# Kernel optimization log

Measured on AMD Instinct MI355X. Metric: run time of the kernel, lower is better.

Reference implementation:

```python
import jax, jax.numpy as jnp
import numpy as np

B, NCLS, NHEADS, CIN, CPROJ = 2, 24, 8, 1024, 128
D0, H0, W0 = 4, 6, 8
KS, EPS = 4, 1e-5


def _bn_relu(x, g, b):
    # training-mode BatchNorm3d (biased var over N,D,H,W) + ReLU
    m = x.mean((0, 2, 3, 4), keepdims=True)
    v = x.var((0, 2, 3, 4), keepdims=True)
    y = (x - m) * jax.lax.rsqrt(v + EPS)
    y = y * g[None, :, None, None, None] + b[None, :, None, None, None]
    return jax.nn.relu(y)


def _convt(x, w, b):
    # torch ConvTranspose3d(k=4, stride=2, pad=1); w: [Cin, Cout, 4,4,4]
    wf = jnp.flip(w, (2, 3, 4)).transpose(1, 0, 2, 3, 4)  # -> [Cout, Cin, k,k,k]
    y = jax.lax.conv_general_dilated(
        x, wf, window_strides=(1, 1, 1),
        padding=[(KS - 1 - 1, KS - 1 - 1)] * 3,  # k-1-p = 2
        lhs_dilation=(2, 2, 2),
        dimension_numbers=("NCDHW", "OIDHW", "NCDHW"))
    return y + b[None, :, None, None, None]


def setup_inputs() -> dict:
    key = jax.random.key(0)
    ks = jax.random.split(key, 20)
    f32 = jnp.float32
    inp = {
        "x_in": jax.random.normal(ks[0], (B, CIN, D0, H0, W0), f32),
        "y_in": jax.random.normal(ks[1], (B, NCLS), f32),
        # multi-headed lookup tables: [n_heads, n_classes, 1*1*1*Cin*Cout]
        "tables": jax.random.normal(ks[2], (NHEADS, NCLS, CIN * CPROJ), f32) * 0.02,
        # BN affine params (gamma init 1, beta init 0 like torch)
        "g0": jnp.ones((1024,), f32), "be0": jnp.zeros((1024,), f32),
        "g1": jnp.ones((512,), f32), "be1": jnp.zeros((512,), f32),
        "g2": jnp.ones((256,), f32), "be2": jnp.zeros((256,), f32),
        "g3": jnp.ones((128,), f32), "be3": jnp.zeros((128,), f32),
        "g4": jnp.ones((32,), f32), "be4": jnp.zeros((32,), f32),
        # ConvTranspose3d weights [Cin, Cout, k, k, k] and biases
        "w1": jax.random.normal(ks[3], (1024, 512, KS, KS, KS), f32) * 0.01,
        "b1": jnp.zeros((512,), f32),
        "w2": jax.random.normal(ks[4], (512, 256, KS, KS, KS), f32) * 0.01,
        "b2": jnp.zeros((256,), f32),
        "w3": jax.random.normal(ks[5], (256, 128, KS, KS, KS), f32) * 0.01,
        "b3": jnp.zeros((128,), f32),
        "w4": jax.random.normal(ks[6], (128, 32, KS, KS, KS), f32) * 0.01,
        "b4": jnp.zeros((32,), f32),
        "w5": jax.random.normal(ks[7], (32, 1, KS, KS, KS), f32) * 0.01,
        "b5": jnp.zeros((1,), f32),
    }
    return inp


def reference(x_in, y_in, tables, g0, be0, g1, be1, g2, be2, g3, be3, g4, be4,
              w1, b1, w2, b2, w3, b3, w4, b4, w5, b5):
    # hypernetwork: per-sample per-head 1x1x1 conv weights
    w = jnp.einsum("bq,hqk->bhk", y_in, tables)
    w = w.reshape(B, NHEADS, CPROJ, CIN)  # [B,H,Cout,Cin]
    # dynamic 1x1x1 conv3d over all samples/heads in one batched contraction
    x = jnp.einsum("bcxyz,bhoc->bhoxyz", x_in, w)
    x = x.reshape(B, NHEADS * CPROJ, D0, H0, W0)  # heads concatenated on channels
    # decoder stack
    x = _bn_relu(x, g0, be0)
    x = _convt(x, w1, b1)
    x = _bn_relu(x, g1, be1)
    x = _convt(x, w2, b2)
    x = _bn_relu(x, g2, be2)
    x = _convt(x, w3, b3)
    x = _bn_relu(x, g3, be3)
    x = _convt(x, w4, b4)
    x = _bn_relu(x, g4, be4)
    x = _convt(x, w5, b5)
    return jax.nn.sigmoid(x)  # [B, 1, 128, 192, 256]
```

## Files before the change

kernel.cpp:

```cpp
#include <hip/hip_runtime.h>
#include <hip/hip_bf16.h>
#include <math.h>

typedef __attribute__((ext_vector_type(8))) short short8;
typedef __attribute__((ext_vector_type(4))) float f32x4;

__device__ __forceinline__ unsigned short f2bf(float f) {
    unsigned u = __builtin_bit_cast(unsigned, f);
    return (unsigned short)((u + 0x7fffu + ((u >> 16) & 1u)) >> 16);
}
__device__ __forceinline__ float bf2f(unsigned short h) {
    unsigned u = ((unsigned)h) << 16;
    return __builtin_bit_cast(float, u);
}

static constexpr int NCLS_ = 24;

__global__ void hyper_k(const float* __restrict__ y, const float* __restrict__ tables,
                        float* __restrict__ wproj) {
    int idx = blockIdx.x * 256 + threadIdx.x;
    int h = idx >> 17;
    int k = idx & 131071;
    const float* t = tables + (size_t)h * NCLS_ * 131072 + k;
    float a0 = 0.f, a1 = 0.f;
#pragma unroll
    for (int q = 0; q < NCLS_; q++) {
        float v = t[(size_t)q << 17];
        a0 = fmaf(y[q], v, a0);
        a1 = fmaf(y[NCLS_ + q], v, a1);
    }
    wproj[idx] = a0;
    wproj[(1u << 20) + idx] = a1;
}

__global__ void conv0_k(const float* __restrict__ xin, const float* __restrict__ wp,
                        unsigned short* __restrict__ x0) {
    int o = blockIdx.x, b = blockIdx.y;
    __shared__ float wl[1024];
    for (int i = threadIdx.x; i < 1024; i += 256)
        wl[i] = wp[((size_t)b << 20) + (size_t)o * 1024 + i];
    __syncthreads();
    int s = threadIdx.x;
    if (s < 192) {
        const float* xb = xin + (size_t)b * 1024 * 192 + s;
        float acc = 0.f;
#pragma unroll 8
        for (int c = 0; c < 1024; c++) acc = fmaf(xb[(size_t)c * 192], wl[c], acc);
        int z = s / 48, rem = s - z * 48, yy = rem / 8, xx = rem - yy * 8;
        int pi = ((z & 1) << 2) | ((yy & 1) << 1) | (xx & 1);
        int qi = ((z >> 1) * 3 + (yy >> 1)) * 4 + (xx >> 1);
        x0[(((size_t)pi * 2 + b) * 24 + qi) * 1024 + o] = f2bf(acc);
    }
}

template <int CO, int CI>
__global__ void wt_k(const float* __restrict__ W, unsigned short* __restrict__ Wt) {
    int t = blockIdx.x * 256 + threadIdx.x;
    int p = t / (CO * CI);
    int rem = t - p * (CO * CI);
    int co = rem / CI;
    int rem2 = rem - co * CI;
    int ci_hi = rem2 >> 3, j = rem2 & 7;
    int pz = p >> 2, py = (p >> 1) & 1, px = p & 1;
    int jz = j >> 2, jy = (j >> 1) & 1, jx = j & 1;
    int tap = (1 - pz + 2 * jz) * 16 + (1 - py + 2 * jy) * 4 + (1 - px + 2 * jx);
    short8 ov;
#pragma unroll
    for (int cl = 0; cl < 8; cl++) {
        float v = W[((size_t)(ci_hi * 8 + cl) * CO + co) * 64 + tap];
        ov[cl] = (short)f2bf(v);
    }
    *(short8*)(Wt + ((size_t)(p * CO + co) * (CI * 8) + ci_hi * 64 + j * 8)) = ov;
}

template <int C>
__global__ __launch_bounds__(256) void bnstats3_k(const unsigned short* __restrict__ x,
                                                  float* __restrict__ sums, int R) {
    constexpr int G = C / 8;
    constexpr int REP = 256 / G;
    const int t = threadIdx.x;
    const int g = t % G;
    const int rep = t / G;
    float s1[8], s2[8];
#pragma unroll
    for (int k = 0; k < 8; k++) { s1[k] = 0.f; s2[k] = 0.f; }
    for (int r = blockIdx.x * REP + rep; r < R; r += gridDim.x * REP) {
        short8 v = *(const short8*)(x + (size_t)r * C + g * 8);
#pragma unroll
        for (int k = 0; k < 8; k++) {
            float f = bf2f((unsigned short)v[k]);
            s1[k] += f;
            s2[k] = fmaf(f, f, s2[k]);
        }
    }
    __shared__ float red[2][256][8];
#pragma unroll
    for (int k = 0; k < 8; k++) { red[0][t][k] = s1[k]; red[1][t][k] = s2[k]; }
    __syncthreads();
#pragma unroll
    for (int step = 128; step >= 1; step >>= 1) {
        if (step >= G) {
            if (t < step) {
#pragma unroll
                for (int k = 0; k < 8; k++) {
                    red[0][t][k] += red[0][t + step][k];
                    red[1][t][k] += red[1][t + step][k];
                }
            }
            __syncthreads();
        }
    }
    if (t < G) {
#pragma unroll
        for (int k = 0; k < 8; k++) {
            atomicAdd(&sums[t * 8 + k], red[0][t][k]);
            atomicAdd(&sums[C + t * 8 + k], red[1][t][k]);
        }
    }
}

__global__ void bnfinal_k(const float* __restrict__ sums, const float* __restrict__ g,
                          const float* __restrict__ be, float* __restrict__ sc,
                          float* __restrict__ sh, int C, float invN) {
    int c = blockIdx.x * 256 + threadIdx.x;
    if (c < C) {
        float m = sums[c] * invN;
        float v = sums[C + c] * invN - m * m;
        float s = g[c] * rsqrtf(v + 1e-5f);
        sc[c] = s;
        sh[c] = be[c] - m * s;
    }
}

__global__ void bnapply2_k(unsigned short* __restrict__ x, const float* __restrict__ sc,
                           const float* __restrict__ sh, int C, int total8) {
    int i = blockIdx.x * 256 + threadIdx.x;
    if (i >= total8) return;
    int c0 = (i * 8) % C;
    short8 v = *(short8*)(x + (size_t)i * 8);
    short8 ov;
#pragma unroll
    for (int k = 0; k < 8; k++) {
        float f = bf2f((unsigned short)v[k]);
        f = fmaxf(0.f, fmaf(f, sc[c0 + k], sh[c0 + k]));
        ov[k] = (short)f2bf(f);
    }
    *(short8*)(x + (size_t)i * 8) = ov;
}

template <int CO, int CI, int DI, int HI, int WI, int TZ, int TY, int TX, int WM, int BMW, bool SIG>
__global__ __launch_bounds__(256) void convt_mfma(const unsigned short* __restrict__ xin,
                                                  const unsigned short* __restrict__ Wt,
                                                  const float* __restrict__ bias,
                                                  void* __restrict__ xout) {
    constexpr int WN = 4 / WM;
    constexpr int WTZ = TZ / WN, WTY = TY, WTX = TX;
    constexpr int LWTX = (WTX == 8) ? 3 : ((WTX == 4) ? 2 : 1);
    constexpr int LWTY = (WTY == 4) ? 2 : ((WTY == 2) ? 1 : 0);
    constexpr int YS = TX + 1;
    constexpr int ZS = (TY + 1) * (TX + 1);
    constexpr int WINR = (TZ + 1) * ZS;
    constexpr int AROWS = WM * BMW;
    constexpr int MT = (CO + BMW * WM - 1) / (BMW * WM);
    constexpr int MF = BMW / 16;
    constexpr int KT = CI / 8;
    constexpr int HH = HI / 2, WH = WI / 2;
    constexpr int SQI = (DI / 2) * HH * WH;
    constexpr int SQO = DI * HI * WI;
    constexpr int WITER = (WINR + 255) / 256;
    constexpr int AITER = (AROWS * 8 + 255) / 256;

    __shared__ short lw[WINR * 8];
    __shared__ short la[AROWS * 72];

    const int tid = threadIdx.x;
    const int mt = blockIdx.x % MT;
    const int nt = blockIdx.x / MT;
    constexpr int NTX = WI / TX, NTY = HI / TY;
    const int tx = nt % NTX;
    const int tyz = nt / NTX;
    const int ty = tyz % NTY;
    const int tz = tyz / NTY;
    const int q0z = tz * TZ, q0y = ty * TY, q0x = tx * TX;
    const int p = blockIdx.y;
    const int pz = p >> 2, py = (p >> 1) & 1, px = p & 1;
    const int b = blockIdx.z;

    const unsigned short* srcp[WITER];
    int dstw[WITER];
#pragma unroll
    for (int rr = 0; rr < WITER; rr++) {
        int row = tid + rr * 256;
        srcp[rr] = nullptr;
        dstw[rr] = row * 8;
        if (row < WINR) {
            int wz = row / ZS;
            int rm = row - wz * ZS;
            int wy = rm / YS;
            int wx = rm - wy * YS;
            int gz = q0z + pz - 1 + wz, gy = q0y + py - 1 + wy, gx = q0x + px - 1 + wx;
            if ((unsigned)gz < (unsigned)DI && (unsigned)gy < (unsigned)HI &&
                (unsigned)gx < (unsigned)WI) {
                int pin = ((gz & 1) << 2) | ((gy & 1) << 1) | (gx & 1);
                int qin = ((gz >> 1) * HH + (gy >> 1)) * WH + (gx >> 1);
                srcp[rr] = xin + (((size_t)pin * 2 + b) * SQI + qin) * CI;
            }
        }
    }
    const unsigned short* asrc[AITER];
    int dsta[AITER];
#pragma unroll
    for (int ar = 0; ar < AITER; ar++) {
        int t2 = tid + ar * 256;
        asrc[ar] = nullptr;
        dsta[ar] = 0;
        if (t2 < AROWS * 8) {
            int row = t2 >> 3, seg = t2 & 7;
            int co = mt * (BMW * WM) + row;
            dsta[ar] = row * 72 + seg * 8;
            if (co < CO) asrc[ar] = Wt + (size_t)(p * CO + co) * (CI * 8) + seg * 8;
        }
    }

    const int lane = tid & 63;
    const int r15 = lane & 15, l4 = lane >> 4;
    const int w = tid >> 6;
    const int wm = (WM == 4) ? w : 0;
    const int wn = (WM == 4) ? 0 : w;
    const int jy = (l4 >> 1) & 1, jx = l4 & 1;

    int baddr[4];
#pragma unroll
    for (int nf = 0; nf < 4; nf++) {
        int n = nf * 16 + r15;
        int qx = n & (WTX - 1);
        int qy = (n >> LWTX) & (WTY - 1);
        int qz = (n >> (LWTX + LWTY)) + wn * WTZ;
        baddr[nf] = ((qz + 1) * ZS + (qy + 1 - jy) * YS + (qx + 1 - jx)) * 8;
    }

    f32x4 acc[MF][4];
#pragma unroll
    for (int mf = 0; mf < MF; mf++) {
        int cobase = mt * (BMW * WM) + wm * BMW + mf * 16 + l4 * 4;
        f32x4 bv;
#pragma unroll
        for (int r = 0; r < 4; r++) bv[r] = (cobase + r < CO) ? bias[cobase + r] : 0.f;
#pragma unroll
        for (int nf = 0; nf < 4; nf++) acc[mf][nf] = bv;
    }

    for (int kt = 0; kt < KT; kt++) {
        __syncthreads();
#pragma unroll
        for (int rr = 0; rr < WITER; rr++) {
            int row = tid + rr * 256;
            if ((WINR % 256 == 0) || row < WINR) {
                short8 v = {0, 0, 0, 0, 0, 0, 0, 0};
                if (srcp[rr]) v = *(const short8*)(srcp[rr] + kt * 8);
                *(short8*)(lw + dstw[rr]) = v;
            }
        }
#pragma unroll
        for (int ar = 0; ar < AITER; ar++) {
            int t2 = tid + ar * 256;
            if (((AROWS * 8) % 256 == 0) || t2 < AROWS * 8) {
                short8 v = {0, 0, 0, 0, 0, 0, 0, 0};
                if (asrc[ar]) v = *(const short8*)(asrc[ar] + kt * 64);
                *(short8*)(la + dsta[ar]) = v;
            }
        }
        __syncthreads();

        short8 af[MF][2], bfr[4][2];
#pragma unroll
        for (int mf = 0; mf < MF; mf++)
#pragma unroll
            for (int ks = 0; ks < 2; ks++)
                af[mf][ks] =
                    *(const short8*)(la + (wm * BMW + mf * 16 + r15) * 72 + ks * 32 + l4 * 8);
#pragma unroll
        for (int nf = 0; nf < 4; nf++)
#pragma unroll
            for (int ks = 0; ks < 2; ks++)
                bfr[nf][ks] = *(const short8*)(lw + baddr[nf] - ks * (ZS * 8));
#pragma unroll
        for (int mf = 0; mf < MF; mf++)
#pragma unroll
            for (int nf = 0; nf < 4; nf++)
#pragma unroll
                for (int ks = 0; ks < 2; ks++)
                    acc[mf][nf] = __builtin_amdgcn_mfma_f32_16x16x32_bf16(
                        af[mf][ks], bfr[nf][ks], acc[mf][nf], 0, 0, 0);
    }

#pragma unroll
    for (int nf = 0; nf < 4; nf++) {
        int n = nf * 16 + r15;
        int qx = q0x + (n & (WTX - 1));
        int qy = q0y + ((n >> LWTX) & (WTY - 1));
        int qz = q0z + (n >> (LWTX + LWTY)) + wn * WTZ;
        if constexpr (SIG) {
            if (l4 == 0) {
                int oz = 2 * qz + pz, oy = 2 * qy + py, ox = 2 * qx + px;
                float v = acc[0][nf][0];
                v = 1.f / (1.f + __expf(-v));
                ((float*)xout)[(size_t)b * (8 * SQO) + ((size_t)oz * (2 * HI) + oy) * (2 * WI) +
                               ox] = v;
            }
        } else {
            int gq = (qz * HI + qy) * WI + qx;
#pragma unroll
            for (int mf = 0; mf < MF; mf++) {
                int cobase = mt * (BMW * WM) + wm * BMW + mf * 16 + l4 * 4;
                unsigned long long pk = 0;
#pragma unroll
                for (int r = 0; r < 4; r++)
                    pk |= (unsigned long long)f2bf(acc[mf][nf][r]) << (16 * r);
                *(unsigned long long*)((unsigned short*)xout +
                                       (((size_t)p * 2 + b) * SQO + gq) * CO + cobase) = pk;
            }
        }
    }
}

extern "C" void kernel_launch(void* const* d_in, const int* in_sizes, int n_in,
                              void* d_out, int out_size, void* d_ws, size_t ws_size,
                              hipStream_t stream) {
    const float* x_in = (const float*)d_in[0];
    const float* y_in = (const float*)d_in[1];
    const float* tables = (const float*)d_in[2];
    const float* g0 = (const float*)d_in[3];
    const float* be0 = (const float*)d_in[4];
    const float* g1 = (const float*)d_in[5];
    const float* be1 = (const float*)d_in[6];
    const float* g2 = (const float*)d_in[7];
    const float* be2 = (const float*)d_in[8];
    const float* g3 = (const float*)d_in[9];
    const float* be3 = (const float*)d_in[10];
    const float* g4 = (const float*)d_in[11];
    const float* be4 = (const float*)d_in[12];
    const float* w1 = (const float*)d_in[13];
    const float* b1 = (const float*)d_in[14];
    const float* w2 = (const float*)d_in[15];
    const float* b2 = (const float*)d_in[16];
    const float* w3 = (const float*)d_in[17];
    const float* b3 = (const float*)d_in[18];
    const float* w4 = (const float*)d_in[19];
    const float* b4 = (const float*)d_in[20];
    const float* w5 = (const float*)d_in[21];
    const float* b5 = (const float*)d_in[22];
    float* out = (float*)d_out;

    char* base = (char*)d_ws;
    size_t off = 0;
    auto alloc = [&](size_t bytes) -> void* {
        void* r = base + off;
        off += (bytes + 255) & ~(size_t)255;
        return r;
    };
    float* wproj = (float*)alloc(8388608);
    unsigned short* x0 = (unsigned short*)alloc(786432);
    unsigned short* x1 = (unsigned short*)alloc(3145728);
    unsigned short* x2 = (unsigned short*)alloc(12582912);
    unsigned short* x3 = (unsigned short*)alloc(50331648);
    unsigned short* x4 = (unsigned short*)alloc(100663296);
    unsigned short* Wt1 = (unsigned short*)alloc(67108864);
    unsigned short* Wt2 = (unsigned short*)alloc(16777216);
    unsigned short* Wt3 = (unsigned short*)alloc(4194304);
    unsigned short* Wt4 = (unsigned short*)alloc(524288);
    unsigned short* Wt5 = (unsigned short*)alloc(4096);
    float* sums = (float*)alloc(8192);
    float* sc = (float*)alloc(4096);
    float* sh = (float*)alloc(4096);

    hyper_k<<<4096, 256, 0, stream>>>(y_in, tables, wproj);
    conv0_k<<<dim3(1024, 2), 256, 0, stream>>>(x_in, wproj, x0);

    wt_k<512, 1024><<<16384, 256, 0, stream>>>(w1, Wt1);
    wt_k<256, 512><<<4096, 256, 0, stream>>>(w2, Wt2);
    wt_k<128, 256><<<1024, 256, 0, stream>>>(w3, Wt3);
    wt_k<32, 128><<<128, 256, 0, stream>>>(w4, Wt4);
    wt_k<1, 32><<<1, 256, 0, stream>>>(w5, Wt5);

    hipMemsetAsync(sums, 0, 2 * 1024 * 4, stream);
    bnstats3_k<1024><<<192, 256, 0, stream>>>(x0, sums, 384);
    bnfinal_k<<<4, 256, 0, stream>>>(sums, g0, be0, sc, sh, 1024, 1.f / 384);
    bnapply2_k<<<192, 256, 0, stream>>>(x0, sc, sh, 1024, 49152);
    convt_mfma<512, 1024, 4, 6, 8, 4, 2, 8, 4, 32, false>
        <<<dim3(12, 8, 2), 256, 0, stream>>>(x0, Wt1, b1, x1);

    hipMemsetAsync(sums, 0, 2 * 512 * 4, stream);
    bnstats3_k<512><<<512, 256, 0, stream>>>(x1, sums, 3072);
    bnfinal_k<<<2, 256, 0, stream>>>(sums, g1, be1, sc, sh, 512, 1.f / 3072);
    bnapply2_k<<<768, 256, 0, stream>>>(x1, sc, sh, 512, 196608);
    convt_mfma<256, 512, 8, 12, 16, 8, 4, 8, 1, 32, false>
        <<<dim3(48, 8, 2), 256, 0, stream>>>(x1, Wt2, b2, x2);

    hipMemsetAsync(sums, 0, 2 * 256 * 4, stream);
    bnstats3_k<256><<<512, 256, 0, stream>>>(x2, sums, 24576);
    bnfinal_k<<<1, 256, 0, stream>>>(sums, g2, be2, sc, sh, 256, 1.f / 24576);
    bnapply2_k<<<3072, 256, 0, stream>>>(x2, sc, sh, 256, 786432);
    convt_mfma<128, 256, 16, 24, 32, 8, 4, 8, 1, 32, false>
        <<<dim3(192, 8, 2), 256, 0, stream>>>(x2, Wt3, b3, x3);

    hipMemsetAsync(sums, 0, 2 * 128 * 4, stream);
    bnstats3_k<128><<<512, 256, 0, stream>>>(x3, sums, 196608);
    bnfinal_k<<<1, 256, 0, stream>>>(sums, g3, be3, sc, sh, 128, 1.f / 196608);
    bnapply2_k<<<12288, 256, 0, stream>>>(x3, sc, sh, 128, 3145728);
    convt_mfma<32, 128, 32, 48, 64, 8, 4, 8, 1, 32, false>
        <<<dim3(384, 8, 2), 256, 0, stream>>>(x3, Wt4, b4, x4);

    hipMemsetAsync(sums, 0, 2 * 32 * 4, stream);
    bnstats3_k<32><<<512, 256, 0, stream>>>(x4, sums, 1572864);
    bnfinal_k<<<1, 256, 0, stream>>>(sums, g4, be4, sc, sh, 32, 1.f / 1572864);
    bnapply2_k<<<24576, 256, 0, stream>>>(x4, sc, sh, 32, 6291456);
    convt_mfma<1, 32, 64, 96, 128, 8, 4, 8, 1, 16, true>
        <<<dim3(3072, 8, 2), 256, 0, stream>>>(x4, Wt5, b5, out);
}
```

Measured before the change: 2.283 ms.

## Add all-parity convt kernel sharing one input window for the last two layers

Adds convt_mfma2, which stages a single halo input window (TZ+2 x TY+2 x TX+2 voxels, 8 channels per step) into LDS and has each of the four waves compute two of the eight output parities from it. Before, each parity was a separate grid slice that reloaded its own input. Layers 4 and 5 now use this kernel, which is aimed at the redundant input reads and the launch overhead of per-parity blocks. In exchange it syncs twice per 8-channel K step with tiny LDS stages, and the final sigmoid layer still wastes most of each MFMA on a single output channel.

```diff
diff --git a/kernel.cpp b/kernel.cpp
--- a/kernel.cpp
+++ b/kernel.cpp
@@ -300,25 +300,170 @@
         int qx = q0x + (n & (WTX - 1));
         int qy = q0y + ((n >> LWTX) & (WTY - 1));
         int qz = q0z + (n >> (LWTX + LWTY)) + wn * WTZ;
-        if constexpr (SIG) {
-            if (l4 == 0) {
-                int oz = 2 * qz + pz, oy = 2 * qy + py, ox = 2 * qx + px;
-                float v = acc[0][nf][0];
-                v = 1.f / (1.f + __expf(-v));
-                ((float*)xout)[(size_t)b * (8 * SQO) + ((size_t)oz * (2 * HI) + oy) * (2 * WI) +
-                               ox] = v;
-            }
-        } else {
-            int gq = (qz * HI + qy) * WI + qx;
+        int gq = (qz * HI + qy) * WI + qx;
+#pragma unroll
+        for (int mf = 0; mf < MF; mf++) {
+            int cobase = mt * (BMW * WM) + wm * BMW + mf * 16 + l4 * 4;
+            unsigned long long pk = 0;
+#pragma unroll
+            for (int r = 0; r < 4; r++)
+                pk |= (unsigned long long)f2bf(acc[mf][nf][r]) << (16 * r);
+            *(unsigned long long*)((unsigned short*)xout +
+                                   (((size_t)p * 2 + b) * SQO + gq) * CO + cobase) = pk;
+        }
+    }
+}
+
+template <int CO, int CI, int DI, int HI, int WI, int TZ, int TY, int TX, int BM, bool SIG>
+__global__ __launch_bounds__(256) void convt_mfma2(const unsigned short* __restrict__ xin,
+                                                   const unsigned short* __restrict__ Wt,
+                                                   const float* __restrict__ bias,
+                                                   void* __restrict__ xout) {
+    constexpr int WZ = TZ + 2, WY = TY + 2, WX = TX + 2;
+    constexpr int WINR = WZ * WY * WX;
+    constexpr int TQ = TZ * TY * TX;
+    constexpr int SF = TQ / 16;
+    constexpr int MF = BM / 16;
+    constexpr int MT = (CO + BM - 1) / BM;
+    constexpr int KT = CI / 8;
+    constexpr int HH = HI / 2, WH = WI / 2;
+    constexpr int SQI = (DI / 2) * HH * WH;
+    constexpr int SQO = DI * HI * WI;
+    static_assert(WINR <= 256, "window must fit one staging pass");
+
+    __shared__ short lw[WINR * 8];
+
+    const int tid = threadIdx.x;
+    const int bx = blockIdx.x;
+    const int mt = bx % MT;
+    const int tile = bx / MT;
+    constexpr int NTX = WI / TX, NTY = HI / TY;
+    const int tx = tile % NTX;
+    const int tyz = tile / NTX;
+    const int ty = tyz % NTY;
+    const int tz = tyz / NTY;
+    const int b = blockIdx.y;
+
+    const unsigned short* srcw = nullptr;
+    if (tid < WINR) {
+        int wz = tid / (WY * WX);
+        int rm = tid - wz * (WY * WX);
+        int wy = rm / WX;
+        int wx = rm - wy * WX;
+        int gz = tz * TZ - 1 + wz, gy = ty * TY - 1 + wy, gx = tx * TX - 1 + wx;
+        if ((unsigned)gz < (unsigned)DI && (unsigned)gy < (unsigned)HI &&
+            (unsigned)gx < (unsigned)WI) {
+            int pin = ((gz & 1) << 2) | ((gy & 1) << 1) | (gx & 1);
+            int qin = ((gz >> 1) * HH + (gy >> 1)) * WH + (gx >> 1);
+            srcw = xin + (((size_t)pin * 2 + b) * SQI + qin) * CI;
+        }
+    }
+
+    const int lane = tid & 63;
+    const int r15 = lane & 15, l4 = lane >> 4;
+    const int w = tid >> 6;
+    const int jy = (l4 >> 1) & 1, jx = l4 & 1;
+
+    const unsigned short* aptr[2][MF];
+#pragma unroll
+    for (int pp = 0; pp < 2; pp++) {
+        int p = 2 * w + pp;
+#pragma unroll
+        for (int mf = 0; mf < MF; mf++) {
+            int co = mt * BM + mf * 16 + r15;
+            if (co >= CO) co = CO - 1;
+            aptr[pp][mf] = Wt + ((size_t)p * CO + co) * (CI * 8) + l4 * 8;
+        }
+    }
+
+    int poff[2];
+#pragma unroll
+    for (int pp = 0; pp < 2; pp++) {
+        int p = 2 * w + pp;
+        poff[pp] = ((p >> 2) * WY + ((p >> 1) & 1)) * WX + (p & 1);
+    }
+    int baddr0[SF];
+#pragma unroll
+    for (int sf = 0; sf < SF; sf++) {
+        int s = sf * 16 + r15;
+        int qxr = s % TX, qyr = (s / TX) % TY, qzr = s / (TX * TY);
+        baddr0[sf] = ((qzr + 1) * WY + (qyr + 1 - jy)) * WX + (qxr + 1 - jx);
+    }
+
+    f32x4 acc[MF][2 * SF];
+#pragma unroll
+    for (int mf = 0; mf < MF; mf++) {
+        int cobase = mt * BM + mf * 16 + l4 * 4;
+        f32x4 bv;
+#pragma unroll
+        for (int r = 0; r < 4; r++) bv[r] = (cobase + r < CO) ? bias[cobase + r] : 0.f;
+#pragma unroll
+        for (int nf = 0; nf < 2 * SF; nf++) acc[mf][nf] = bv;
+    }
+
+    for (int kt = 0; kt < KT; kt++) {
+        __syncthreads();
+        if (tid < WINR) {
+            short8 v = {0, 0, 0, 0, 0, 0, 0, 0};
+            if (srcw) v = *(const short8*)(srcw + kt * 8);
+            *(short8*)(lw + tid * 8) = v;
+        }
+        short8 af[2][MF][2];
+#pragma unroll
+        for (int pp = 0; pp < 2; pp++)
 #pragma unroll
             for (int mf = 0; mf < MF; mf++) {
-                int cobase = mt * (BMW * WM) + wm * BMW + mf * 16 + l4 * 4;
-                unsigned long long pk = 0;
-#pragma unroll
-                for (int r = 0; r < 4; r++)
-                    pk |= (unsigned long long)f2bf(acc[mf][nf][r]) << (16 * r);
-                *(unsigned long long*)((unsigned short*)xout +
-                                       (((size_t)p * 2 + b) * SQO + gq) * CO + cobase) = pk;
+                const unsigned short* ap = aptr[pp][mf] + kt * 64;
+                af[pp][mf][0] = *(const short8*)(ap);
+                af[pp][mf][1] = *(const short8*)(ap + 32);
+            }
+        __syncthreads();
+#pragma unroll
+        for (int pp = 0; pp < 2; pp++)
+#pragma unroll
+            for (int sf = 0; sf < SF; sf++) {
+                short8 b0 = *(const short8*)(lw + (baddr0[sf] + poff[pp]) * 8);
+                short8 b1 = *(const short8*)(lw + (baddr0[sf] + poff[pp] - WY * WX) * 8);
+#pragma unroll
+                for (int mf = 0; mf < MF; mf++) {
+                    acc[mf][pp * SF + sf] = __builtin_amdgcn_mfma_f32_16x16x32_bf16(
+                        af[pp][mf][0], b0, acc[mf][pp * SF + sf], 0, 0, 0);
+                    acc[mf][pp * SF + sf] = __builtin_amdgcn_mfma_f32_16x16x32_bf16(
+                        af[pp][mf][1], b1, acc[mf][pp * SF + sf], 0, 0, 0);
+                }
+            }
+    }
+
+#pragma unroll
+    for (int pp = 0; pp < 2; pp++) {
+        int p = 2 * w + pp;
+        int pz = p >> 2, py = (p >> 1) & 1, px = p & 1;
+#pragma unroll
+        for (int sf = 0; sf < SF; sf++) {
+            int s = sf * 16 + r15;
+            int qx = tx * TX + s % TX;
+            int qy = ty * TY + (s / TX) % TY;
+            int qz = tz * TZ + s / (TX * TY);
+            if constexpr (SIG) {
+                if (l4 == 0) {
+                    int oz = 2 * qz + pz, oy = 2 * qy + py, ox = 2 * qx + px;
+                    float v = acc[0][pp * SF + sf][0];
+                    v = 1.f / (1.f + __expf(-v));
+                    ((float*)xout)[(size_t)b * (8 * SQO) +
+                                   ((size_t)oz * (2 * HI) + oy) * (2 * WI) + ox] = v;
+                }
+            } else {
+                int gq = (qz * HI + qy) * WI + qx;
+#pragma unroll
+                for (int mf = 0; mf < MF; mf++) {
+                    int cobase = mt * BM + mf * 16 + l4 * 4;
+                    unsigned long long pk = 0;
+#pragma unroll
+                    for (int r = 0; r < 4; r++)
+                        pk |= (unsigned long long)f2bf(acc[mf][pp * SF + sf][r]) << (16 * r);
+                    *(unsigned long long*)((unsigned short*)xout +
+                                           (((size_t)p * 2 + b) * SQO + gq) * CO + cobase) = pk;
+                }
             }
         }
     }
@@ -408,13 +553,13 @@
     bnstats3_k<128><<<512, 256, 0, stream>>>(x3, sums, 196608);
     bnfinal_k<<<1, 256, 0, stream>>>(sums, g3, be3, sc, sh, 128, 1.f / 196608);
     bnapply2_k<<<12288, 256, 0, stream>>>(x3, sc, sh, 128, 3145728);
-    convt_mfma<32, 128, 32, 48, 64, 8, 4, 8, 1, 32, false>
-        <<<dim3(384, 8, 2), 256, 0, stream>>>(x3, Wt4, b4, x4);
+    convt_mfma2<32, 128, 32, 48, 64, 2, 4, 8, 32, false>
+        <<<dim3(1536, 2), 256, 0, stream>>>(x3, Wt4, b4, x4);
 
     hipMemsetAsync(sums, 0, 2 * 32 * 4, stream);
     bnstats3_k<32><<<512, 256, 0, stream>>>(x4, sums, 1572864);
     bnfinal_k<<<1, 256, 0, stream>>>(sums, g4, be4, sc, sh, 32, 1.f / 1572864);
     bnapply2_k<<<24576, 256, 0, stream>>>(x4, sc, sh, 32, 6291456);
-    convt_mfma<1, 32, 64, 96, 128, 8, 4, 8, 1, 16, true>
-        <<<dim3(3072, 8, 2), 256, 0, stream>>>(x4, Wt5, b5, out);
-}
+    convt_mfma2<1, 32, 64, 96, 128, 2, 4, 8, 16, true>
+        <<<dim3(12288, 2), 256, 0, stream>>>(x4, Wt5, b5, out);
+}
```

Result: faster. 2.016 ms (-11.7%).
